# Kernel tuning notes

Hardware: AMD Instinct MI355X
Metric: run time of the kernel (lower is better)

The kernel has to match this reference:

```python
import jax, jax.numpy as jnp
import numpy as np

D_OUT = 64  # out_embed_size, also the softmax scale base

def setup_inputs() -> dict:
    key = jax.random.key(0)
    kx, kk, kq, kv = jax.random.split(key, 4)
    B, T, C = 8, 2048, 768
    x = jax.random.normal(kx, (B, T, C), dtype=jnp.float32)
    # torch Linear weights are [out, in]; store as [in, out] for x @ W
    s = 1.0 / np.sqrt(C)
    Wk = jax.random.uniform(kk, (C, D_OUT), jnp.float32, -s, s)
    Wq = jax.random.uniform(kq, (C, D_OUT), jnp.float32, -s, s)
    Wv = jax.random.uniform(kv, (C, D_OUT), jnp.float32, -s, s)
    return {"x": x, "Wq": Wq, "Wk": Wk, "Wv": Wv}

def reference(x, Wq, Wk, Wv):
    B, T, C = x.shape
    q = x @ Wq  # [B,T,D]
    k = x @ Wk
    v = x @ Wv
    scale = D_OUT ** -0.5
    qk = jnp.einsum('btd,bsd->bts', q, k) * scale  # [B,T,T]
    causal = jnp.tril(jnp.ones((T, T), dtype=bool))
    qk = jnp.where(causal, qk, -jnp.inf)
    attn = jax.nn.softmax(qk, axis=-1)
    # dropout p=0.0 -> identity
    return jnp.einsum('bts,bsd->btd', attn, v)
```

## Files before the change

kernel.cpp:

```cpp
#include <hip/hip_runtime.h>
#include <hip/hip_bf16.h>

#define BB 8
#define TT 2048
#define CC 768
#define DD 64
#define BT (BB * TT)

typedef __attribute__((ext_vector_type(8))) short bf16x8;
typedef __attribute__((ext_vector_type(4))) float f32x4;

__device__ __forceinline__ unsigned short f2b(float f) {
  unsigned u = __builtin_bit_cast(unsigned, f);
  u += 0x7fffu + ((u >> 16) & 1u);
  return (unsigned short)(u >> 16);
}

__device__ __forceinline__ bf16x8 pack8(float4 a, float4 b) {
  unsigned short t[8] = {f2b(a.x), f2b(a.y), f2b(a.z), f2b(a.w),
                         f2b(b.x), f2b(b.y), f2b(b.z), f2b(b.w)};
  return *reinterpret_cast<bf16x8*>(t);
}

__device__ __forceinline__ void gl16(const void* g, void* l) {
  __builtin_amdgcn_global_load_lds(
      (const __attribute__((address_space(1))) unsigned int*)g,
      (__attribute__((address_space(3))) unsigned int*)l, 16, 0, 0);
}

#define RAW_BAR()                                \
  do {                                           \
    asm volatile("" ::: "memory");               \
    __builtin_amdgcn_s_barrier();                \
    asm volatile("" ::: "memory");               \
  } while (0)

__global__ __launch_bounds__(256) void wt_kernel(const float* __restrict__ Wq,
                                                 const float* __restrict__ Wk,
                                                 const float* __restrict__ Wv,
                                                 unsigned short* __restrict__ wt) {
  int tid = blockIdx.x * 256 + threadIdx.x;
  if (tid >= 192 * 96) return;
  int k0 = (tid % 96) * 8;
  int c = tid / 96;
  const float* W = (c < 64) ? Wq : (c < 128 ? Wk : Wv);
  int cc = c & 63;
  unsigned short t[8];
#pragma unroll
  for (int e = 0; e < 8; ++e) t[e] = f2b(W[(k0 + e) * 64 + cc]);
  *reinterpret_cast<bf16x8*>(&wt[c * 768 + k0]) = *reinterpret_cast<bf16x8*>(t);
}

__global__ __launch_bounds__(512, 2) void proj_kernel(const float* __restrict__ x,
                                                      const unsigned short* __restrict__ wt,
                                                      unsigned short* __restrict__ qws,
                                                      unsigned short* __restrict__ kws,
                                                      unsigned short* __restrict__ vtws) {
  __shared__ __align__(16) float xl[2][32 * 64];
  __shared__ __align__(16) unsigned short wl[2][192 * 64];

  const int tid = threadIdx.x;
  const int wv = tid >> 6;
  const int l = tid & 63;
  const int lo = l & 15, hi = l >> 4;
  const int rg = wv & 1;
  const int cq = wv >> 1;
  const int m0 = blockIdx.x * 32;

  const int xrow = tid >> 4;
  const int xcs = ((tid & 15) ^ (xrow & 7)) * 4;
  const float* xsrc = x + (size_t)(m0 + xrow) * 768 + xcs;
  const int xdst = (tid & ~63) * 4;

  f32x4 acc[3];
#pragma unroll
  for (int i = 0; i < 3; ++i) acc[i] = (f32x4){0.f, 0.f, 0.f, 0.f};

  auto stage = [&](int buf, int k0) {
    gl16(xsrc + k0, &xl[buf][xdst]);
#pragma unroll
    for (int it = 0; it < 3; ++it) {
      int ch = tid + it * 512;
      int row = ch >> 3;
      int c = ((ch & 7) ^ (row & 7)) * 8;
      gl16(wt + row * 768 + k0 + c, &wl[buf][(ch & ~63) * 8]);
    }
  };

  stage(0, 0);

  const int arow = rg * 16 + lo;
  const int ax = arow & 7;
  int buf = 0;
  for (int step = 0; step < 12; ++step) {
    if (step < 11) {
      stage(buf ^ 1, (step + 1) * 64);
      asm volatile("s_waitcnt vmcnt(4)" ::: "memory");
    } else {
      asm volatile("s_waitcnt vmcnt(0)" ::: "memory");
    }
    __builtin_amdgcn_s_barrier();
    __builtin_amdgcn_sched_barrier(0);

    const float* xb = xl[buf];
    const unsigned short* wb = wl[buf];
    float4 a0 = *reinterpret_cast<const float4*>(&xb[arow * 64 + ((hi * 2 + 0) ^ ax) * 4]);
    float4 a1 = *reinterpret_cast<const float4*>(&xb[arow * 64 + ((hi * 2 + 1) ^ ax) * 4]);
    float4 a2 = *reinterpret_cast<const float4*>(&xb[arow * 64 + ((8 + hi * 2 + 0) ^ ax) * 4]);
    float4 a3 = *reinterpret_cast<const float4*>(&xb[arow * 64 + ((8 + hi * 2 + 1) ^ ax) * 4]);
    bf16x8 af0 = pack8(a0, a1);
    bf16x8 af1 = pack8(a2, a3);
    __builtin_amdgcn_s_setprio(1);
#pragma unroll
    for (int ct = 0; ct < 3; ++ct) {
      int cr = cq * 48 + ct * 16 + lo;
      int cx = cr & 7;
      bf16x8 b0 = *reinterpret_cast<const bf16x8*>(&wb[cr * 64 + ((hi) ^ cx) * 8]);
      bf16x8 b1 = *reinterpret_cast<const bf16x8*>(&wb[cr * 64 + ((4 + hi) ^ cx) * 8]);
      acc[ct] = __builtin_amdgcn_mfma_f32_16x16x32_bf16(af0, b0, acc[ct], 0, 0, 0);
      acc[ct] = __builtin_amdgcn_mfma_f32_16x16x32_bf16(af1, b1, acc[ct], 0, 0, 0);
    }
    __builtin_amdgcn_s_setprio(0);
    RAW_BAR();
    buf ^= 1;
  }

  const float QS = 0.125f * 1.4426950408889634f;
#pragma unroll
  for (int ct = 0; ct < 3; ++ct) {
    const int c = cq * 48 + ct * 16 + lo;
    const int mat = c >> 6;
    const int cc = c & 63;
#pragma unroll
    for (int r = 0; r < 4; ++r) {
      const int m = m0 + rg * 16 + hi * 4 + r;
      float val = acc[ct][r];
      if (mat == 0) {
        qws[m * 64 + cc] = f2b(val * QS);
      } else if (mat == 1) {
        kws[m * 64 + cc] = f2b(val);
      } else {
        vtws[(size_t)((m >> 11) * 64 + cc) * 2048 + (m & 2047)] = f2b(val);
      }
    }
  }
}

__global__ __launch_bounds__(256) void attn_kernel(const unsigned short* __restrict__ qws,
                                                   const unsigned short* __restrict__ kws,
                                                   const unsigned short* __restrict__ vtws,
                                                   float* __restrict__ out) {
  __shared__ __align__(16) unsigned short Kl[2][128 * 64];
  __shared__ __align__(16) unsigned short Vl[2][64 * 128];
  __shared__ __align__(16) unsigned short Pl[4][16 * 140];

  const int tid = threadIdx.x;
  const int wv = tid >> 6;
  const int l = tid & 63;
  const int lo = l & 15, hi = l >> 4;
  const int b = blockIdx.x & 7;
  const int u = blockIdx.x >> 3;
  const int t0 = u * 64 + wv * 16;
  const int nt = (u >> 1) + 1;

  const unsigned short* qb = qws + (size_t)b * TT * DD;
  const unsigned short* kb = kws + (size_t)b * TT * DD;
  const unsigned short* vb = vtws + (size_t)b * DD * TT;
  unsigned short* Plw = &Pl[wv][0];

  const bf16x8 qf0 = *reinterpret_cast<const bf16x8*>(&qb[(t0 + lo) * 64 + hi * 8]);
  const bf16x8 qf1 = *reinterpret_cast<const bf16x8*>(&qb[(t0 + lo) * 64 + 32 + hi * 8]);

  auto stage = [&](int buf, int kv0) {
#pragma unroll
    for (int it = 0; it < 4; ++it) {
      int ch = tid + it * 256;
      int kr = ch >> 3;
      int kc = ((ch & 7) ^ (kr & 7)) * 8;
      gl16(kb + (size_t)(kv0 + kr) * 64 + kc, &Kl[buf][(ch & ~63) * 8]);
      int vd = ch >> 4;
      int vc = ((ch & 15) ^ (vd & 7)) * 8;
      gl16(vb + (size_t)vd * 2048 + kv0 + vc, &Vl[buf][(ch & ~63) * 8]);
    }
  };

  f32x4 Oa[4];
#pragma unroll
  for (int m = 0; m < 4; ++m) Oa[m] = (f32x4){0.f, 0.f, 0.f, 0.f};
  float srow[4] = {0.f, 0.f, 0.f, 0.f};

  stage(0, 0);

  const int kx = lo & 7;
  int buf = 0;
  for (int j = 0; j < nt; ++j) {
    if (j + 1 < nt) {
      stage(buf ^ 1, (j + 1) * 128);
      asm volatile("s_waitcnt vmcnt(8)" ::: "memory");
    } else {
      asm volatile("s_waitcnt vmcnt(0)" ::: "memory");
    }
    __builtin_amdgcn_s_barrier();
    __builtin_amdgcn_sched_barrier(0);

    const unsigned short* Kb = &Kl[buf][0];
    const unsigned short* Vb = &Vl[buf][0];

    f32x4 S[8];
    __builtin_amdgcn_s_setprio(1);
#pragma unroll
    for (int n = 0; n < 8; ++n) {
      const int key = n * 16 + lo;
      bf16x8 k0f = *reinterpret_cast<const bf16x8*>(&Kb[key * 64 + ((hi) ^ kx) * 8]);
      bf16x8 k1f = *reinterpret_cast<const bf16x8*>(&Kb[key * 64 + ((4 + hi) ^ kx) * 8]);
      S[n] = (f32x4){0.f, 0.f, 0.f, 0.f};
      S[n] = __builtin_amdgcn_mfma_f32_16x16x32_bf16(qf0, k0f, S[n], 0, 0, 0);
      S[n] = __builtin_amdgcn_mfma_f32_16x16x32_bf16(qf1, k1f, S[n], 0, 0, 0);
    }
    __builtin_amdgcn_s_setprio(0);

    if (j == nt - 1) {
#pragma unroll
      for (int n = 0; n < 8; ++n) {
        const int kg = j * 128 + n * 16 + lo;
#pragma unroll
        for (int r = 0; r < 4; ++r) {
          if (kg > t0 + hi * 4 + r) S[n][r] = -1e30f;
        }
      }
    }

#pragma unroll
    for (int n = 0; n < 8; ++n)
#pragma unroll
      for (int r = 0; r < 4; ++r) {
        float p = exp2f(S[n][r]);
        srow[r] += p;
        Plw[(hi * 4 + r) * 140 + n * 16 + lo] = f2b(p);
      }

    bf16x8 pa0 = *reinterpret_cast<const bf16x8*>(&Plw[lo * 140 + hi * 8]);
    bf16x8 pa1 = *reinterpret_cast<const bf16x8*>(&Plw[lo * 140 + 32 + hi * 8]);
    bf16x8 pa2 = *reinterpret_cast<const bf16x8*>(&Plw[lo * 140 + 64 + hi * 8]);
    bf16x8 pa3 = *reinterpret_cast<const bf16x8*>(&Plw[lo * 140 + 96 + hi * 8]);

    __builtin_amdgcn_s_setprio(1);
#pragma unroll
    for (int m = 0; m < 4; ++m) {
      const int d = m * 16 + lo;
      const int dx = d & 7;
      bf16x8 v0 = *reinterpret_cast<const bf16x8*>(&Vb[d * 128 + ((hi + 0) ^ dx) * 8]);
      bf16x8 v1 = *reinterpret_cast<const bf16x8*>(&Vb[d * 128 + ((hi + 4) ^ dx) * 8]);
      bf16x8 v2 = *reinterpret_cast<const bf16x8*>(&Vb[d * 128 + ((hi + 8) ^ dx) * 8]);
      bf16x8 v3 = *reinterpret_cast<const bf16x8*>(&Vb[d * 128 + ((hi + 12) ^ dx) * 8]);
      Oa[m] = __builtin_amdgcn_mfma_f32_16x16x32_bf16(pa0, v0, Oa[m], 0, 0, 0);
      Oa[m] = __builtin_amdgcn_mfma_f32_16x16x32_bf16(pa1, v1, Oa[m], 0, 0, 0);
      Oa[m] = __builtin_amdgcn_mfma_f32_16x16x32_bf16(pa2, v2, Oa[m], 0, 0, 0);
      Oa[m] = __builtin_amdgcn_mfma_f32_16x16x32_bf16(pa3, v3, Oa[m], 0, 0, 0);
    }
    __builtin_amdgcn_s_setprio(0);

    RAW_BAR();
    buf ^= 1;
  }

#pragma unroll
  for (int r = 0; r < 4; ++r) {
    float v = srow[r];
    v += __shfl_xor(v, 1);
    v += __shfl_xor(v, 2);
    v += __shfl_xor(v, 4);
    v += __shfl_xor(v, 8);
    srow[r] = 1.0f / v;
  }

  float* ob = out + ((size_t)b * TT + t0) * 64;
#pragma unroll
  for (int m = 0; m < 4; ++m)
#pragma unroll
    for (int r = 0; r < 4; ++r)
      ob[(hi * 4 + r) * 64 + m * 16 + lo] = Oa[m][r] * srow[r];
}

extern "C" void kernel_launch(void* const* d_in, const int* in_sizes, int n_in,
                              void* d_out, int out_size, void* d_ws, size_t ws_size,
                              hipStream_t stream) {
  const float* x = (const float*)d_in[0];
  const float* Wq = (const float*)d_in[1];
  const float* Wk = (const float*)d_in[2];
  const float* Wv = (const float*)d_in[3];
  float* out = (float*)d_out;

  char* ws = (char*)d_ws;
  unsigned short* qws = (unsigned short*)(ws);
  unsigned short* kws = (unsigned short*)(ws + (size_t)2 * 1024 * 1024);
  unsigned short* vtws = (unsigned short*)(ws + (size_t)4 * 1024 * 1024);
  unsigned short* wt = (unsigned short*)(ws + (size_t)6 * 1024 * 1024);

  hipLaunchKernelGGL(wt_kernel, dim3(72), dim3(256), 0, stream, Wq, Wk, Wv, wt);
  hipLaunchKernelGGL(proj_kernel, dim3(BT / 32), dim3(512), 0, stream, x, wt, qws, kws, vtws);
  hipLaunchKernelGGL(attn_kernel, dim3(256), dim3(256), 0, stream, qws, kws, vtws, out);
}
```

Baseline: 143.8 us.

## Restructure attention into single-wave blocks with register-prefetched K/V tiles

Measured after the change: 142.5 us. About the same (-0.9%).

```diff
diff --git a/kernel.cpp b/kernel.cpp
--- a/kernel.cpp
+++ b/kernel.cpp
@@ -146,140 +146,126 @@
   }
 }
 
-__global__ __launch_bounds__(256) void attn_kernel(const unsigned short* __restrict__ qws,
-                                                   const unsigned short* __restrict__ kws,
-                                                   const unsigned short* __restrict__ vtws,
-                                                   float* __restrict__ out) {
-  __shared__ __align__(16) unsigned short Kl[2][128 * 64];
-  __shared__ __align__(16) unsigned short Vl[2][64 * 128];
-  __shared__ __align__(16) unsigned short Pl[4][16 * 140];
-
-  const int tid = threadIdx.x;
-  const int wv = tid >> 6;
-  const int l = tid & 63;
+__global__ __launch_bounds__(64) void attn_kernel(const unsigned short* __restrict__ qws,
+                                                  const unsigned short* __restrict__ kws,
+                                                  const unsigned short* __restrict__ vtws,
+                                                  float* __restrict__ out) {
+  __shared__ __align__(16) unsigned int Pl32[16 * 40];
+
+  const int l = threadIdx.x;
   const int lo = l & 15, hi = l >> 4;
   const int b = blockIdx.x & 7;
-  const int u = blockIdx.x >> 3;
-  const int t0 = u * 64 + wv * 16;
-  const int nt = (u >> 1) + 1;
+  const int tloc = 127 - (blockIdx.x >> 3);
+  const int t0 = tloc * 16;
+  const int nt = (tloc >> 2) + 1;
+  const unsigned xw = (lo & 3) << 2;
 
   const unsigned short* qb = qws + (size_t)b * TT * DD;
   const unsigned short* kb = kws + (size_t)b * TT * DD;
   const unsigned short* vb = vtws + (size_t)b * DD * TT;
-  unsigned short* Plw = &Pl[wv][0];
 
   const bf16x8 qf0 = *reinterpret_cast<const bf16x8*>(&qb[(t0 + lo) * 64 + hi * 8]);
   const bf16x8 qf1 = *reinterpret_cast<const bf16x8*>(&qb[(t0 + lo) * 64 + 32 + hi * 8]);
 
-  auto stage = [&](int buf, int kv0) {
-#pragma unroll
-    for (int it = 0; it < 4; ++it) {
-      int ch = tid + it * 256;
-      int kr = ch >> 3;
-      int kc = ((ch & 7) ^ (kr & 7)) * 8;
-      gl16(kb + (size_t)(kv0 + kr) * 64 + kc, &Kl[buf][(ch & ~63) * 8]);
-      int vd = ch >> 4;
-      int vc = ((ch & 15) ^ (vd & 7)) * 8;
-      gl16(vb + (size_t)vd * 2048 + kv0 + vc, &Vl[buf][(ch & ~63) * 8]);
-    }
-  };
+  const unsigned short* kp = kb + (size_t)lo * 64 + hi * 8;
+  const unsigned short* vp = vb + (size_t)lo * 2048 + hi * 8;
 
   f32x4 Oa[4];
 #pragma unroll
   for (int m = 0; m < 4; ++m) Oa[m] = (f32x4){0.f, 0.f, 0.f, 0.f};
-  float srow[4] = {0.f, 0.f, 0.f, 0.f};
-
-  stage(0, 0);
-
-  const int kx = lo & 7;
-  int buf = 0;
+  float srow = 0.f;
+
+  bf16x8 kc[8], vc[8];
+#pragma unroll
+  for (int n = 0; n < 4; ++n) {
+    kc[2 * n + 0] = *reinterpret_cast<const bf16x8*>(kp + (size_t)(n * 16) * 64);
+    kc[2 * n + 1] = *reinterpret_cast<const bf16x8*>(kp + (size_t)(n * 16) * 64 + 32);
+  }
+#pragma unroll
+  for (int m = 0; m < 4; ++m) {
+    vc[2 * m + 0] = *reinterpret_cast<const bf16x8*>(vp + (size_t)m * 16 * 2048);
+    vc[2 * m + 1] = *reinterpret_cast<const bf16x8*>(vp + (size_t)m * 16 * 2048 + 32);
+  }
+
   for (int j = 0; j < nt; ++j) {
-    if (j + 1 < nt) {
-      stage(buf ^ 1, (j + 1) * 128);
-      asm volatile("s_waitcnt vmcnt(8)" ::: "memory");
-    } else {
-      asm volatile("s_waitcnt vmcnt(0)" ::: "memory");
-    }
-    __builtin_amdgcn_s_barrier();
+    const bool pf = (j + 1 < nt);
+    bf16x8 kn[8], vn[8];
+    if (pf) {
+      const size_t kvo = (size_t)(j + 1) * 64;
+#pragma unroll
+      for (int n = 0; n < 4; ++n) {
+        kn[2 * n + 0] = *reinterpret_cast<const bf16x8*>(kp + (kvo + n * 16) * 64);
+        kn[2 * n + 1] = *reinterpret_cast<const bf16x8*>(kp + (kvo + n * 16) * 64 + 32);
+      }
+#pragma unroll
+      for (int m = 0; m < 4; ++m) {
+        vn[2 * m + 0] = *reinterpret_cast<const bf16x8*>(vp + (size_t)m * 16 * 2048 + kvo);
+        vn[2 * m + 1] = *reinterpret_cast<const bf16x8*>(vp + (size_t)m * 16 * 2048 + kvo + 32);
+      }
+    }
     __builtin_amdgcn_sched_barrier(0);
 
-    const unsigned short* Kb = &Kl[buf][0];
-    const unsigned short* Vb = &Vl[buf][0];
-
-    f32x4 S[8];
+    f32x4 S[4];
     __builtin_amdgcn_s_setprio(1);
 #pragma unroll
-    for (int n = 0; n < 8; ++n) {
-      const int key = n * 16 + lo;
-      bf16x8 k0f = *reinterpret_cast<const bf16x8*>(&Kb[key * 64 + ((hi) ^ kx) * 8]);
-      bf16x8 k1f = *reinterpret_cast<const bf16x8*>(&Kb[key * 64 + ((4 + hi) ^ kx) * 8]);
+    for (int n = 0; n < 4; ++n) {
       S[n] = (f32x4){0.f, 0.f, 0.f, 0.f};
-      S[n] = __builtin_amdgcn_mfma_f32_16x16x32_bf16(qf0, k0f, S[n], 0, 0, 0);
-      S[n] = __builtin_amdgcn_mfma_f32_16x16x32_bf16(qf1, k1f, S[n], 0, 0, 0);
+      S[n] = __builtin_amdgcn_mfma_f32_16x16x32_bf16(kc[2 * n + 0], qf0, S[n], 0, 0, 0);
+      S[n] = __builtin_amdgcn_mfma_f32_16x16x32_bf16(kc[2 * n + 1], qf1, S[n], 0, 0, 0);
     }
     __builtin_amdgcn_s_setprio(0);
 
     if (j == nt - 1) {
 #pragma unroll
-      for (int n = 0; n < 8; ++n) {
-        const int kg = j * 128 + n * 16 + lo;
-#pragma unroll
-        for (int r = 0; r < 4; ++r) {
-          if (kg > t0 + hi * 4 + r) S[n][r] = -1e30f;
-        }
-      }
-    }
-
-#pragma unroll
-    for (int n = 0; n < 8; ++n)
-#pragma unroll
-      for (int r = 0; r < 4; ++r) {
-        float p = exp2f(S[n][r]);
-        srow[r] += p;
-        Plw[(hi * 4 + r) * 140 + n * 16 + lo] = f2b(p);
-      }
-
-    bf16x8 pa0 = *reinterpret_cast<const bf16x8*>(&Plw[lo * 140 + hi * 8]);
-    bf16x8 pa1 = *reinterpret_cast<const bf16x8*>(&Plw[lo * 140 + 32 + hi * 8]);
-    bf16x8 pa2 = *reinterpret_cast<const bf16x8*>(&Plw[lo * 140 + 64 + hi * 8]);
-    bf16x8 pa3 = *reinterpret_cast<const bf16x8*>(&Plw[lo * 140 + 96 + hi * 8]);
+      for (int n = 0; n < 4; ++n)
+#pragma unroll
+        for (int r = 0; r < 4; ++r)
+          if (j * 64 + n * 16 + hi * 4 + r > t0 + lo) S[n][r] = -1e30f;
+    }
+
+#pragma unroll
+    for (int n = 0; n < 4; ++n) {
+      float p0, p1, p2, p3;
+      asm("v_exp_f32 %0, %1" : "=v"(p0) : "v"(S[n][0]));
+      asm("v_exp_f32 %0, %1" : "=v"(p1) : "v"(S[n][1]));
+      asm("v_exp_f32 %0, %1" : "=v"(p2) : "v"(S[n][2]));
+      asm("v_exp_f32 %0, %1" : "=v"(p3) : "v"(S[n][3]));
+      srow += (p0 + p1) + (p2 + p3);
+      unsigned w0, w1;
+      asm("v_cvt_pk_bf16_f32 %0, %1, %2" : "=v"(w0) : "v"(p0), "v"(p1));
+      asm("v_cvt_pk_bf16_f32 %0, %1, %2" : "=v"(w1) : "v"(p2), "v"(p3));
+      *reinterpret_cast<uint2*>(&Pl32[lo * 40 + ((n * 8 + hi * 2) ^ xw)]) =
+          make_uint2(w0, w1);
+    }
+    bf16x8 pa0 = *reinterpret_cast<const bf16x8*>(&Pl32[lo * 40 + ((hi * 4) ^ xw)]);
+    bf16x8 pa1 = *reinterpret_cast<const bf16x8*>(&Pl32[lo * 40 + ((16 + hi * 4) ^ xw)]);
 
     __builtin_amdgcn_s_setprio(1);
 #pragma unroll
     for (int m = 0; m < 4; ++m) {
-      const int d = m * 16 + lo;
-      const int dx = d & 7;
-      bf16x8 v0 = *reinterpret_cast<const bf16x8*>(&Vb[d * 128 + ((hi + 0) ^ dx) * 8]);
-      bf16x8 v1 = *reinterpret_cast<const bf16x8*>(&Vb[d * 128 + ((hi + 4) ^ dx) * 8]);
-      bf16x8 v2 = *reinterpret_cast<const bf16x8*>(&Vb[d * 128 + ((hi + 8) ^ dx) * 8]);
-      bf16x8 v3 = *reinterpret_cast<const bf16x8*>(&Vb[d * 128 + ((hi + 12) ^ dx) * 8]);
-      Oa[m] = __builtin_amdgcn_mfma_f32_16x16x32_bf16(pa0, v0, Oa[m], 0, 0, 0);
-      Oa[m] = __builtin_amdgcn_mfma_f32_16x16x32_bf16(pa1, v1, Oa[m], 0, 0, 0);
-      Oa[m] = __builtin_amdgcn_mfma_f32_16x16x32_bf16(pa2, v2, Oa[m], 0, 0, 0);
-      Oa[m] = __builtin_amdgcn_mfma_f32_16x16x32_bf16(pa3, v3, Oa[m], 0, 0, 0);
+      Oa[m] = __builtin_amdgcn_mfma_f32_16x16x32_bf16(pa0, vc[2 * m + 0], Oa[m], 0, 0, 0);
+      Oa[m] = __builtin_amdgcn_mfma_f32_16x16x32_bf16(pa1, vc[2 * m + 1], Oa[m], 0, 0, 0);
     }
     __builtin_amdgcn_s_setprio(0);
 
-    RAW_BAR();
-    buf ^= 1;
-  }
-
+    if (pf) {
+#pragma unroll
+      for (int i = 0; i < 8; ++i) { kc[i] = kn[i]; vc[i] = vn[i]; }
+    }
+  }
+
+  float v = srow;
+  v += __shfl_xor(v, 16);
+  v += __shfl_xor(v, 32);
+
+  float* ob = out + ((size_t)b * TT + t0) * 64;
 #pragma unroll
   for (int r = 0; r < 4; ++r) {
-    float v = srow[r];
-    v += __shfl_xor(v, 1);
-    v += __shfl_xor(v, 2);
-    v += __shfl_xor(v, 4);
-    v += __shfl_xor(v, 8);
-    srow[r] = 1.0f / v;
-  }
-
-  float* ob = out + ((size_t)b * TT + t0) * 64;
-#pragma unroll
-  for (int m = 0; m < 4; ++m)
-#pragma unroll
-    for (int r = 0; r < 4; ++r)
-      ob[(hi * 4 + r) * 64 + m * 16 + lo] = Oa[m][r] * srow[r];
+    const float inv = 1.0f / __shfl(v, hi * 4 + r);
+#pragma unroll
+    for (int m = 0; m < 4; ++m)
+      ob[(hi * 4 + r) * 64 + m * 16 + lo] = Oa[m][r] * inv;
+  }
 }
 
 extern "C" void kernel_launch(void* const* d_in, const int* in_sizes, int n_in,
@@ -299,5 +285,5 @@
 
   hipLaunchKernelGGL(wt_kernel, dim3(72), dim3(256), 0, stream, Wq, Wk, Wv, wt);
   hipLaunchKernelGGL(proj_kernel, dim3(BT / 32), dim3(512), 0, stream, x, wt, qws, kws, vtws);
-  hipLaunchKernelGGL(attn_kernel, dim3(256), dim3(256), 0, stream, qws, kws, vtws, out);
-}
+  hipLaunchKernelGGL(attn_kernel, dim3(1024), dim3(64), 0, stream, qws, kws, vtws, out);
+}
```
